# Optimization experiments

Measured on AMD Instinct MI355X. Metric: run time of the kernel, lower is better.

Reference implementation:

```python
import jax, jax.numpy as jnp
import numpy as np

T, H, I, E = 8192, 1024, 2816, 8


def setup_inputs() -> dict:
    key = jax.random.key(0)
    ks = jax.random.split(key, 4)
    x = jax.random.normal(ks[0], (T, H), dtype=jnp.float32)
    router_logits = jax.random.normal(ks[1], (T, E), dtype=jnp.float32)
    # params scaled like trained weights
    w13 = jax.random.normal(ks[2], (E, 2 * I, H), dtype=jnp.float32) * (1.0 / np.sqrt(H))
    w2 = jax.random.normal(ks[3], (E, H, I), dtype=jnp.float32) * (1.0 / np.sqrt(I))
    return {"x": x, "router_logits": router_logits, "w13": w13, "w2": w2, "top_k": 2}


def reference(x, router_logits, w13, w2, top_k):
    """select_experts (softmax scoring, top-k, renormalize) + fused_experts (SiLU-gated MLP per expert, weighted combine)."""
    Ttok, Hd = x.shape
    Ex, twoI, _ = w13.shape
    Id = twoI // 2
    # --- router: softmax -> top_k -> renormalize ---
    probs = jax.nn.softmax(router_logits.astype(jnp.float32), axis=-1)  # [T, E]
    topk_w, topk_ids = jax.lax.top_k(probs, top_k)                      # [T, k]
    topk_w = topk_w / jnp.sum(topk_w, axis=-1, keepdims=True)
    # per-expert combine weight matrix [T, E] (scatter of topk weights)
    comb = jnp.zeros((Ttok, Ex), dtype=x.dtype).at[
        jnp.arange(Ttok)[:, None], topk_ids
    ].add(topk_w.astype(x.dtype))
    # --- expert MLPs: out = sum_e comb[:,e] * (silu(x W1_e^T) * (x W3_e^T)) W2_e^T ---
    out = jnp.zeros_like(x)
    for e in range(Ex):  # small fixed expert count
        gate = x @ w13[e, :Id].T          # [T, I]
        up = x @ w13[e, Id:].T            # [T, I]
        h = jax.nn.silu(gate) * up        # [T, I]
        out = out + comb[:, e:e + 1] * (h @ w2[e].T)  # [T, H]
    return out
```

## Files before the change

### kernel.cpp

```cpp
#include <hip/hip_runtime.h>
#include <hip/hip_bf16.h>

#define T_TOK 8192
#define H_DIM 1024
#define I_DIM 2816
#define E_NUM 8
#define R_TOT (2 * T_TOK)

typedef __hip_bfloat16 bf16;
typedef __attribute__((ext_vector_type(8))) short short8;
typedef __attribute__((ext_vector_type(4))) float floatx4;

__device__ inline unsigned short f2b(float f) {
    bf16 b = __float2bfloat16(f);
    unsigned short u;
    __builtin_memcpy(&u, &b, 2);
    return u;
}

__device__ inline short8 ld_cvt8(const float* p) {
    float4 f0 = *(const float4*)p;
    float4 f1 = *(const float4*)(p + 4);
    short8 r;
    r[0] = (short)f2b(f0.x); r[1] = (short)f2b(f0.y);
    r[2] = (short)f2b(f0.z); r[3] = (short)f2b(f0.w);
    r[4] = (short)f2b(f1.x); r[5] = (short)f2b(f1.y);
    r[6] = (short)f2b(f1.z); r[7] = (short)f2b(f1.w);
    return r;
}

__device__ inline void gl_lds16(const void* g, void* l) {
    __builtin_amdgcn_global_load_lds(
        (const __attribute__((address_space(1))) void*)g,
        (__attribute__((address_space(3))) void*)l, 16, 0, 0);
}


__global__ __launch_bounds__(256) void cvt_bf16_kernel(const float* __restrict__ in,
                                                       bf16* __restrict__ out, int n8) {
    int stride = gridDim.x * blockDim.x;
    for (int i = blockIdx.x * blockDim.x + threadIdx.x; i < n8; i += stride) {
        short8 v = ld_cvt8(in + (size_t)i * 8);
        *(short8*)(out + (size_t)i * 8) = v;
    }
}


__global__ void zero_counts_kernel(int* counts) {
    if (threadIdx.x < E_NUM) counts[threadIdx.x] = 0;
}

__global__ void zero_out_kernel(float* __restrict__ out) {
    size_t i = ((size_t)blockIdx.x * 256 + threadIdx.x) * 4;
    float4 z = {0.0f, 0.0f, 0.0f, 0.0f};
    *(float4*)(out + i) = z;
}

__global__ void router_kernel(const float* __restrict__ logits,
                              int* __restrict__ topk_id,
                              float* __restrict__ topk_w,
                              int* __restrict__ counts) {
    int t = blockIdx.x * blockDim.x + threadIdx.x;
    if (t >= T_TOK) return;
    float l[E_NUM];
#pragma unroll
    for (int e = 0; e < E_NUM; e++) l[e] = logits[t * E_NUM + e];
    int i0 = 0;
#pragma unroll
    for (int e = 1; e < E_NUM; e++)
        if (l[e] > l[i0]) i0 = e;
    int i1 = (i0 == 0) ? 1 : 0;
#pragma unroll
    for (int e = 0; e < E_NUM; e++) {
        if (e == i0 || e == i1) continue;
        if (l[e] > l[i1]) i1 = e;
    }
    float p1 = __expf(l[i1] - l[i0]);
    float w0 = 1.0f / (1.0f + p1);
    float w1 = p1 / (1.0f + p1);
    topk_id[2 * t] = i0;
    topk_id[2 * t + 1] = i1;
    topk_w[2 * t] = w0;
    topk_w[2 * t + 1] = w1;
    atomicAdd(&counts[i0], 1);
    atomicAdd(&counts[i1], 1);
}

__global__ void offsets_kernel(const int* __restrict__ counts,
                               int* __restrict__ offs,
                               int* __restrict__ cursor) {
    if (threadIdx.x == 0 && blockIdx.x == 0) {
        int acc = 0;
        for (int e = 0; e < E_NUM; e++) {
            offs[e] = acc;
            cursor[e] = acc;
            acc += counts[e];
        }
        offs[E_NUM] = acc;
    }
}

__global__ void scatter_kernel(const int* __restrict__ topk_id,
                               const float* __restrict__ topk_w,
                               int* __restrict__ cursor,
                               int* __restrict__ rowtok,
                               float* __restrict__ wrow) {
    int t = blockIdx.x * blockDim.x + threadIdx.x;
    if (t >= T_TOK) return;
#pragma unroll
    for (int j = 0; j < 2; j++) {
        int e = topk_id[2 * t + j];
        int r = atomicAdd(&cursor[e], 1);
        rowtok[r] = t;
        wrow[r] = topk_w[2 * t + j];
    }
}


__global__ __launch_bounds__(256) void gemm1_bf16_kernel(
    const bf16* __restrict__ xb, const bf16* __restrict__ wptr,
    long long wstride, int e_base,
    const int* __restrict__ offs, const int* __restrict__ rowtok,
    bf16* __restrict__ h) {
    const int ei = blockIdx.y >> 6;
    const int e = e_base + ei;
    const int tm = blockIdx.y & 63;
    const int mBeg = offs[e], mEnd = offs[e + 1];
    const int m0 = mBeg + tm * 128;
    if (m0 >= mEnd) return;
    const int n0 = blockIdx.x * 128;

    __shared__ alignas(16) bf16 As[2][128 * 32];
    __shared__ alignas(16) bf16 Bg[2][128 * 32];
    __shared__ alignas(16) bf16 Bu[2][128 * 32];

    const int tid = threadIdx.x;
    const int lane = tid & 63;
    const int wv = tid >> 6;
    const int wr = wv >> 1, wc = wv & 1;

    const int c0 = tid, c1 = tid + 256;
    const int ar0 = c0 >> 2, ks0 = (c0 & 3) * 8;
    const int ar1 = c1 >> 2, ks1 = (c1 & 3) * 8;
    const bf16* aG0 = xb + (size_t)rowtok[min(m0 + ar0, R_TOT - 1)] * H_DIM + ks0;
    const bf16* aG1 = xb + (size_t)rowtok[min(m0 + ar1, R_TOT - 1)] * H_DIM + ks1;
    const bf16* w13e = wptr + (size_t)ei * wstride;
    const bf16* bG0 = w13e + (size_t)(n0 + ar0) * H_DIM + ks0;
    const bf16* bG1 = w13e + (size_t)(n0 + ar1) * H_DIM + ks1;
    const bf16* uG0 = w13e + (size_t)(I_DIM + n0 + ar0) * H_DIM + ks0;
    const bf16* uG1 = w13e + (size_t)(I_DIM + n0 + ar1) * H_DIM + ks1;

    const int wb8 = (wv * 64) * 8;
    const int wb8b = (wv * 64 + 256) * 8;

#define STG1(B, KT)                          \
    gl_lds16(aG0 + (KT), &As[B][wb8]);       \
    gl_lds16(aG1 + (KT), &As[B][wb8b]);      \
    gl_lds16(bG0 + (KT), &Bg[B][wb8]);       \
    gl_lds16(bG1 + (KT), &Bg[B][wb8b]);      \
    gl_lds16(uG0 + (KT), &Bu[B][wb8]);       \
    gl_lds16(uG1 + (KT), &Bu[B][wb8b]);

    floatx4 accG[4][4] = {};
    floatx4 accU[4][4] = {};

    const int lr = lane & 15;
    const int kg = lane >> 4;

    STG1(0, 0);
    __syncthreads();

    int cur = 0;
    for (int kt = 0; kt < H_DIM; kt += 32) {
        if (kt + 32 < H_DIM) { STG1(cur ^ 1, kt + 32); }

        short8 af[4], bgf[4], buf2[4];
#pragma unroll
        for (int i = 0; i < 4; i++)
            af[i] = *(const short8*)(&As[cur][(wr * 64 + i * 16 + lr) * 32 + kg * 8]);
#pragma unroll
        for (int j = 0; j < 4; j++) {
            bgf[j] = *(const short8*)(&Bg[cur][(wc * 64 + j * 16 + lr) * 32 + kg * 8]);
            buf2[j] = *(const short8*)(&Bu[cur][(wc * 64 + j * 16 + lr) * 32 + kg * 8]);
        }
#pragma unroll
        for (int i = 0; i < 4; i++)
#pragma unroll
            for (int j = 0; j < 4; j++) {
                accG[i][j] = __builtin_amdgcn_mfma_f32_16x16x32_bf16(af[i], bgf[j], accG[i][j], 0, 0, 0);
                accU[i][j] = __builtin_amdgcn_mfma_f32_16x16x32_bf16(af[i], buf2[j], accU[i][j], 0, 0, 0);
            }
        __syncthreads();
        cur ^= 1;
    }
#undef STG1

    const int quad = lane >> 4;
#pragma unroll
    for (int i = 0; i < 4; i++) {
        const int grb = m0 + wr * 64 + i * 16 + quad * 4;
#pragma unroll
        for (int j = 0; j < 4; j++) {
            const int gc = n0 + wc * 64 + j * 16 + lr;
#pragma unroll
            for (int v = 0; v < 4; v++) {
                const int gr = grb + v;
                if (gr < mEnd) {
                    float g = accG[i][j][v];
                    float u = accU[i][j][v];
                    float s = g / (1.0f + __expf(-g));
                    h[(size_t)gr * I_DIM + gc] = __float2bfloat16(s * u);
                }
            }
        }
    }
}


__global__ __launch_bounds__(256) void gemm2_bf16_kernel(
    const bf16* __restrict__ hbuf, const bf16* __restrict__ wptr,
    long long wstride, int e_base,
    const int* __restrict__ offs, const int* __restrict__ rowtok,
    const float* __restrict__ wrow, float* __restrict__ out) {
    const int ei = blockIdx.y >> 6;
    const int e = e_base + ei;
    const int tm = blockIdx.y & 63;
    const int mBeg = offs[e], mEnd = offs[e + 1];
    const int m0 = mBeg + tm * 128;
    if (m0 >= mEnd) return;
    const int n0 = blockIdx.x * 128;

    __shared__ alignas(16) bf16 As[2][128 * 32];
    __shared__ alignas(16) bf16 Bs[2][128 * 32];

    const int tid = threadIdx.x;
    const int lane = tid & 63;
    const int wv = tid >> 6;
    const int wr = wv >> 1, wc = wv & 1;

    const int c0 = tid, c1 = tid + 256;
    const int ar0 = c0 >> 2, ks0 = (c0 & 3) * 8;
    const int ar1 = c1 >> 2, ks1 = (c1 & 3) * 8;
    const bf16* aG0 = hbuf + (size_t)min(m0 + ar0, R_TOT - 1) * I_DIM + ks0;
    const bf16* aG1 = hbuf + (size_t)min(m0 + ar1, R_TOT - 1) * I_DIM + ks1;
    const bf16* w2e = wptr + (size_t)ei * wstride;
    const bf16* bG0 = w2e + (size_t)(n0 + ar0) * I_DIM + ks0;
    const bf16* bG1 = w2e + (size_t)(n0 + ar1) * I_DIM + ks1;

    const int wb8 = (wv * 64) * 8;
    const int wb8b = (wv * 64 + 256) * 8;

#define STG2(B, KT)                          \
    gl_lds16(aG0 + (KT), &As[B][wb8]);       \
    gl_lds16(aG1 + (KT), &As[B][wb8b]);      \
    gl_lds16(bG0 + (KT), &Bs[B][wb8]);       \
    gl_lds16(bG1 + (KT), &Bs[B][wb8b]);

    floatx4 acc[4][4] = {};
    const int lr = lane & 15;
    const int kg = lane >> 4;

    STG2(0, 0);
    __syncthreads();

    int cur = 0;
    for (int kt = 0; kt < I_DIM; kt += 32) {
        if (kt + 32 < I_DIM) { STG2(cur ^ 1, kt + 32); }

        short8 af[4], bf_[4];
#pragma unroll
        for (int i = 0; i < 4; i++)
            af[i] = *(const short8*)(&As[cur][(wr * 64 + i * 16 + lr) * 32 + kg * 8]);
#pragma unroll
        for (int j = 0; j < 4; j++)
            bf_[j] = *(const short8*)(&Bs[cur][(wc * 64 + j * 16 + lr) * 32 + kg * 8]);
#pragma unroll
        for (int i = 0; i < 4; i++)
#pragma unroll
            for (int j = 0; j < 4; j++)
                acc[i][j] = __builtin_amdgcn_mfma_f32_16x16x32_bf16(af[i], bf_[j], acc[i][j], 0, 0, 0);
        __syncthreads();
        cur ^= 1;
    }
#undef STG2

    const int quad = lane >> 4;
#pragma unroll
    for (int i = 0; i < 4; i++) {
        const int grb = m0 + wr * 64 + i * 16 + quad * 4;
#pragma unroll
        for (int j = 0; j < 4; j++) {
            const int gc = n0 + wc * 64 + j * 16 + lr;
#pragma unroll
            for (int v = 0; v < 4; v++) {
                const int gr = grb + v;
                if (gr < mEnd) {
                    const int t = rowtok[gr];
                    atomicAdd(&out[(size_t)t * H_DIM + gc], wrow[gr] * acc[i][j][v]);
                }
            }
        }
    }
}


__global__ __launch_bounds__(256) void gemm1_f32_kernel(
    const float* __restrict__ x, const float* __restrict__ w13,
    const int* __restrict__ offs, const int* __restrict__ rowtok,
    bf16* __restrict__ h) {
    const int e = blockIdx.y >> 6;
    const int tm = blockIdx.y & 63;
    const int mBeg = offs[e], mEnd = offs[e + 1];
    const int m0 = mBeg + tm * 128;
    if (m0 >= mEnd) return;
    const int n0 = blockIdx.x * 128;

    __shared__ alignas(16) bf16 As[128 * 32];
    __shared__ alignas(16) bf16 Bg[128 * 32];
    __shared__ alignas(16) bf16 Bu[128 * 32];

    const int tid = threadIdx.x;
    const int lane = tid & 63;
    const int wv = tid >> 6;
    const int wr = wv >> 1, wc = wv & 1;

    const int c0 = tid, c1 = tid + 256;
    const int ar0 = c0 >> 2, ks0 = (c0 & 3) * 8;
    const int ar1 = c1 >> 2, ks1 = (c1 & 3) * 8;
    const int rr0 = min(m0 + ar0, R_TOT - 1);
    const int rr1 = min(m0 + ar1, R_TOT - 1);
    const float* aG0 = x + (size_t)rowtok[rr0] * H_DIM + ks0;
    const float* aG1 = x + (size_t)rowtok[rr1] * H_DIM + ks1;
    const float* w13e = w13 + (size_t)e * (2 * I_DIM) * H_DIM;
    const float* bG0 = w13e + (size_t)(n0 + ar0) * H_DIM + ks0;
    const float* bG1 = w13e + (size_t)(n0 + ar1) * H_DIM + ks1;
    const float* uG0 = w13e + (size_t)(I_DIM + n0 + ar0) * H_DIM + ks0;
    const float* uG1 = w13e + (size_t)(I_DIM + n0 + ar1) * H_DIM + ks1;

    floatx4 accG[4][4] = {};
    floatx4 accU[4][4] = {};

    const int lr = lane & 15;
    const int kg = lane >> 4;

    for (int kt = 0; kt < H_DIM; kt += 32) {
        short8 va0 = ld_cvt8(aG0 + kt);
        short8 va1 = ld_cvt8(aG1 + kt);
        short8 vg0 = ld_cvt8(bG0 + kt);
        short8 vg1 = ld_cvt8(bG1 + kt);
        short8 vu0 = ld_cvt8(uG0 + kt);
        short8 vu1 = ld_cvt8(uG1 + kt);
        __syncthreads();
        *(short8*)(As + c0 * 8) = va0;
        *(short8*)(As + c1 * 8) = va1;
        *(short8*)(Bg + c0 * 8) = vg0;
        *(short8*)(Bg + c1 * 8) = vg1;
        *(short8*)(Bu + c0 * 8) = vu0;
        *(short8*)(Bu + c1 * 8) = vu1;
        __syncthreads();

        short8 af[4], bgf[4], buf2[4];
#pragma unroll
        for (int i = 0; i < 4; i++)
            af[i] = *(const short8*)(As + (wr * 64 + i * 16 + lr) * 32 + kg * 8);
#pragma unroll
        for (int j = 0; j < 4; j++) {
            bgf[j] = *(const short8*)(Bg + (wc * 64 + j * 16 + lr) * 32 + kg * 8);
            buf2[j] = *(const short8*)(Bu + (wc * 64 + j * 16 + lr) * 32 + kg * 8);
        }
#pragma unroll
        for (int i = 0; i < 4; i++)
#pragma unroll
            for (int j = 0; j < 4; j++) {
                accG[i][j] = __builtin_amdgcn_mfma_f32_16x16x32_bf16(af[i], bgf[j], accG[i][j], 0, 0, 0);
                accU[i][j] = __builtin_amdgcn_mfma_f32_16x16x32_bf16(af[i], buf2[j], accU[i][j], 0, 0, 0);
            }
    }

    const int quad = lane >> 4;
#pragma unroll
    for (int i = 0; i < 4; i++) {
        const int grb = m0 + wr * 64 + i * 16 + quad * 4;
#pragma unroll
        for (int j = 0; j < 4; j++) {
            const int gc = n0 + wc * 64 + j * 16 + lr;
#pragma unroll
            for (int v = 0; v < 4; v++) {
                const int gr = grb + v;
                if (gr < mEnd) {
                    float g = accG[i][j][v];
                    float u = accU[i][j][v];
                    float s = g / (1.0f + __expf(-g));
                    h[(size_t)gr * I_DIM + gc] = __float2bfloat16(s * u);
                }
            }
        }
    }
}

__global__ __launch_bounds__(256) void gemm2_f32_kernel(
    const bf16* __restrict__ hbuf, const float* __restrict__ w2,
    const int* __restrict__ offs, const int* __restrict__ rowtok,
    const float* __restrict__ wrow, float* __restrict__ out) {
    const int e = blockIdx.y >> 6;
    const int tm = blockIdx.y & 63;
    const int mBeg = offs[e], mEnd = offs[e + 1];
    const int m0 = mBeg + tm * 128;
    if (m0 >= mEnd) return;
    const int n0 = blockIdx.x * 128;

    __shared__ alignas(16) bf16 As[128 * 32];
    __shared__ alignas(16) bf16 Bs[128 * 32];

    const int tid = threadIdx.x;
    const int lane = tid & 63;
    const int wv = tid >> 6;
    const int wr = wv >> 1, wc = wv & 1;

    const int c0 = tid, c1 = tid + 256;
    const int ar0 = c0 >> 2, ks0 = (c0 & 3) * 8;
    const int ar1 = c1 >> 2, ks1 = (c1 & 3) * 8;
    const bf16* aG0 = hbuf + (size_t)min(m0 + ar0, R_TOT - 1) * I_DIM + ks0;
    const bf16* aG1 = hbuf + (size_t)min(m0 + ar1, R_TOT - 1) * I_DIM + ks1;
    const float* w2e = w2 + (size_t)e * H_DIM * I_DIM;
    const float* bG0 = w2e + (size_t)(n0 + ar0) * I_DIM + ks0;
    const float* bG1 = w2e + (size_t)(n0 + ar1) * I_DIM + ks1;

    floatx4 acc[4][4] = {};
    const int lr = lane & 15;
    const int kg = lane >> 4;

    for (int kt = 0; kt < I_DIM; kt += 32) {
        short8 va0 = *(const short8*)(aG0 + kt);
        short8 va1 = *(const short8*)(aG1 + kt);
        short8 vb0 = ld_cvt8(bG0 + kt);
        short8 vb1 = ld_cvt8(bG1 + kt);
        __syncthreads();
        *(short8*)(As + c0 * 8) = va0;
        *(short8*)(As + c1 * 8) = va1;
        *(short8*)(Bs + c0 * 8) = vb0;
        *(short8*)(Bs + c1 * 8) = vb1;
        __syncthreads();

        short8 af[4], bf_[4];
#pragma unroll
        for (int i = 0; i < 4; i++)
            af[i] = *(const short8*)(As + (wr * 64 + i * 16 + lr) * 32 + kg * 8);
#pragma unroll
        for (int j = 0; j < 4; j++)
            bf_[j] = *(const short8*)(Bs + (wc * 64 + j * 16 + lr) * 32 + kg * 8);
#pragma unroll
        for (int i = 0; i < 4; i++)
#pragma unroll
            for (int j = 0; j < 4; j++)
                acc[i][j] = __builtin_amdgcn_mfma_f32_16x16x32_bf16(af[i], bf_[j], acc[i][j], 0, 0, 0);
    }

    const int quad = lane >> 4;
#pragma unroll
    for (int i = 0; i < 4; i++) {
        const int grb = m0 + wr * 64 + i * 16 + quad * 4;
#pragma unroll
        for (int j = 0; j < 4; j++) {
            const int gc = n0 + wc * 64 + j * 16 + lr;
#pragma unroll
            for (int v = 0; v < 4; v++) {
                const int gr = grb + v;
                if (gr < mEnd) {
                    const int t = rowtok[gr];
                    atomicAdd(&out[(size_t)t * H_DIM + gc], wrow[gr] * acc[i][j][v]);
                }
            }
        }
    }
}


extern "C" void kernel_launch(void* const* d_in, const int* in_sizes, int n_in,
                              void* d_out, int out_size, void* d_ws, size_t ws_size,
                              hipStream_t stream) {
    const float* x = (const float*)d_in[0];
    const float* rl = (const float*)d_in[1];
    const float* w13 = (const float*)d_in[2];
    const float* w2 = (const float*)d_in[3];
    float* out = (float*)d_out;

    char* ws = (char*)d_ws;
    int* counts = (int*)(ws);
    int* offs = (int*)(ws + 256);
    int* cursor = (int*)(ws + 512);
    int* topk_id = (int*)(ws + 1024);
    float* topk_w = (float*)(ws + 1024 + 65536);
    int* rowtok = (int*)(ws + 1024 + 2 * 65536);
    float* wrow = (float*)(ws + 1024 + 3 * 65536);

    const size_t BASE = 1024 + 4 * 65536;
    const size_t H_BYTES = (size_t)R_TOT * I_DIM * 2;
    const size_t XB_BYTES = (size_t)T_TOK * H_DIM * 2;
    const size_t W13_BYTES = (size_t)E_NUM * 2 * I_DIM * H_DIM * 2;
    const size_t W13_SLICE = (size_t)2 * I_DIM * H_DIM * 2;
    const size_t W2_SLICE = (size_t)H_DIM * I_DIM * 2;

    bf16* h = (bf16*)(ws + BASE);
    bf16* xb = (bf16*)(ws + BASE + H_BYTES);
    bf16* wbuf = (bf16*)(ws + BASE + H_BYTES + XB_BYTES);

    const size_t NEED_BULK = BASE + H_BYTES + XB_BYTES + W13_BYTES;
    const size_t NEED_SLICE = BASE + H_BYTES + XB_BYTES + W13_SLICE;

    zero_out_kernel<<<(T_TOK * H_DIM) / (256 * 4), 256, 0, stream>>>(out);
    zero_counts_kernel<<<1, 64, 0, stream>>>(counts);
    router_kernel<<<(T_TOK + 255) / 256, 256, 0, stream>>>(rl, topk_id, topk_w, counts);
    offsets_kernel<<<1, 64, 0, stream>>>(counts, offs, cursor);
    scatter_kernel<<<(T_TOK + 255) / 256, 256, 0, stream>>>(topk_id, topk_w, cursor, rowtok, wrow);

    if (ws_size >= NEED_BULK) {
        cvt_bf16_kernel<<<2048, 256, 0, stream>>>(x, xb, (T_TOK * H_DIM) / 8);
        cvt_bf16_kernel<<<2048, 256, 0, stream>>>(w13, wbuf, (int)(W13_BYTES / 2 / 8));
        gemm1_bf16_kernel<<<dim3(I_DIM / 128, E_NUM * 64), 256, 0, stream>>>(
            xb, wbuf, (long long)2 * I_DIM * H_DIM, 0, offs, rowtok, h);
        cvt_bf16_kernel<<<2048, 256, 0, stream>>>(w2, wbuf, (E_NUM * H_DIM * I_DIM) / 8);
        gemm2_bf16_kernel<<<dim3(H_DIM / 128, E_NUM * 64), 256, 0, stream>>>(
            h, wbuf, (long long)H_DIM * I_DIM, 0, offs, rowtok, wrow, out);
    } else if (ws_size >= NEED_SLICE) {
        cvt_bf16_kernel<<<2048, 256, 0, stream>>>(x, xb, (T_TOK * H_DIM) / 8);
        for (int e = 0; e < E_NUM; e++) {
            cvt_bf16_kernel<<<1024, 256, 0, stream>>>(
                w13 + (size_t)e * 2 * I_DIM * H_DIM, wbuf, (int)(W13_SLICE / 2 / 8));
            gemm1_bf16_kernel<<<dim3(I_DIM / 128, 64), 256, 0, stream>>>(
                xb, wbuf, 0LL, e, offs, rowtok, h);
        }
        for (int e = 0; e < E_NUM; e++) {
            cvt_bf16_kernel<<<1024, 256, 0, stream>>>(
                w2 + (size_t)e * H_DIM * I_DIM, wbuf, (int)(W2_SLICE / 2 / 8));
            gemm2_bf16_kernel<<<dim3(H_DIM / 128, 64), 256, 0, stream>>>(
                h, wbuf, 0LL, e, offs, rowtok, wrow, out);
        }
    } else {
        gemm1_f32_kernel<<<dim3(I_DIM / 128, E_NUM * 64), 256, 0, stream>>>(
            x, w13, offs, rowtok, h);
        gemm2_f32_kernel<<<dim3(H_DIM / 128, E_NUM * 64), 256, 0, stream>>>(
            h, w2, offs, rowtok, wrow, out);
    }
}
```

Baseline: 1.180 ms.

## Enlarge MoE GEMM tiles to 512-thread blocks with swizzled LDS and phased MFMA

Both expert GEMMs now use 512-thread blocks with larger output tiles: 256x128 for the gate/up GEMM and 256x256 for the down GEMM. K steps go from 32 to 64, and shared memory is a 128KB dynamic buffer with an XOR swizzle to reduce bank conflicts. Each K tile is split into four MFMA phases separated by raw barriers, with s_setprio raised around the MFMA bursts. The aim is more operand reuse per global load and better latency hiding. The cost is higher register and LDS pressure, which means one block per CU, and the down GEMM no longer clamps row indices when reading h.

```diff
diff --git a/kernel.cpp b/kernel.cpp
--- a/kernel.cpp
+++ b/kernel.cpp
@@ -35,6 +35,9 @@
         (__attribute__((address_space(3))) void*)l, 16, 0, 0);
 }
 
+#define BARX() do { asm volatile("" ::: "memory"); __builtin_amdgcn_s_barrier(); asm volatile("" ::: "memory"); } while (0)
+#define WAIT_VM0() asm volatile("s_waitcnt vmcnt(0)" ::: "memory")
+
 
 __global__ __launch_bounds__(256) void cvt_bf16_kernel(const float* __restrict__ in,
                                                        bf16* __restrict__ out, int n8) {
@@ -117,85 +120,102 @@
 }
 
 
-__global__ __launch_bounds__(256) void gemm1_bf16_kernel(
+__global__ __launch_bounds__(512) void gemm1_8ph_kernel(
     const bf16* __restrict__ xb, const bf16* __restrict__ wptr,
     long long wstride, int e_base,
     const int* __restrict__ offs, const int* __restrict__ rowtok,
     bf16* __restrict__ h) {
-    const int ei = blockIdx.y >> 6;
+    const int ei = blockIdx.y >> 5;
     const int e = e_base + ei;
-    const int tm = blockIdx.y & 63;
+    const int tm = blockIdx.y & 31;
     const int mBeg = offs[e], mEnd = offs[e + 1];
-    const int m0 = mBeg + tm * 128;
+    const int m0 = mBeg + tm * 256;
     if (m0 >= mEnd) return;
     const int n0 = blockIdx.x * 128;
 
-    __shared__ alignas(16) bf16 As[2][128 * 32];
-    __shared__ alignas(16) bf16 Bg[2][128 * 32];
-    __shared__ alignas(16) bf16 Bu[2][128 * 32];
+    extern __shared__ char smem[];
+    bf16* Alds = (bf16*)smem;
+    bf16* Gl = Alds + 32768;
+    bf16* Ul = Gl + 16384;
 
     const int tid = threadIdx.x;
     const int lane = tid & 63;
     const int wv = tid >> 6;
     const int wr = wv >> 1, wc = wv & 1;
-
-    const int c0 = tid, c1 = tid + 256;
-    const int ar0 = c0 >> 2, ks0 = (c0 & 3) * 8;
-    const int ar1 = c1 >> 2, ks1 = (c1 & 3) * 8;
-    const bf16* aG0 = xb + (size_t)rowtok[min(m0 + ar0, R_TOT - 1)] * H_DIM + ks0;
-    const bf16* aG1 = xb + (size_t)rowtok[min(m0 + ar1, R_TOT - 1)] * H_DIM + ks1;
+    const int lr = lane & 15, kg = lane >> 4;
+    const int swz = lr & 7;
+    const int srow = wv * 8 + (lane >> 3);
+    const int socto = ((lane & 7) ^ (lane >> 3)) * 8;
+    const int dA = wv * 512;
+
     const bf16* w13e = wptr + (size_t)ei * wstride;
-    const bf16* bG0 = w13e + (size_t)(n0 + ar0) * H_DIM + ks0;
-    const bf16* bG1 = w13e + (size_t)(n0 + ar1) * H_DIM + ks1;
-    const bf16* uG0 = w13e + (size_t)(I_DIM + n0 + ar0) * H_DIM + ks0;
-    const bf16* uG1 = w13e + (size_t)(I_DIM + n0 + ar1) * H_DIM + ks1;
-
-    const int wb8 = (wv * 64) * 8;
-    const int wb8b = (wv * 64 + 256) * 8;
-
-#define STG1(B, KT)                          \
-    gl_lds16(aG0 + (KT), &As[B][wb8]);       \
-    gl_lds16(aG1 + (KT), &As[B][wb8b]);      \
-    gl_lds16(bG0 + (KT), &Bg[B][wb8]);       \
-    gl_lds16(bG1 + (KT), &Bg[B][wb8b]);      \
-    gl_lds16(uG0 + (KT), &Bu[B][wb8]);       \
-    gl_lds16(uG1 + (KT), &Bu[B][wb8b]);
+    const bf16* aP[4];
+    const bf16 *gP[2], *uP[2];
+#pragma unroll
+    for (int L = 0; L < 4; L++)
+        aP[L] = xb + (size_t)rowtok[min(m0 + L * 64 + srow, R_TOT - 1)] * H_DIM + socto;
+#pragma unroll
+    for (int L = 0; L < 2; L++) {
+        gP[L] = w13e + (size_t)(n0 + L * 64 + srow) * H_DIM + socto;
+        uP[L] = w13e + (size_t)(I_DIM + n0 + L * 64 + srow) * H_DIM + socto;
+    }
+
+#define STG1(B, KT) do {                                          \
+    gl_lds16(aP[0] + (KT), Alds + (B) * 16384 + 0 * 4096 + dA);   \
+    gl_lds16(aP[1] + (KT), Alds + (B) * 16384 + 1 * 4096 + dA);   \
+    gl_lds16(aP[2] + (KT), Alds + (B) * 16384 + 2 * 4096 + dA);   \
+    gl_lds16(aP[3] + (KT), Alds + (B) * 16384 + 3 * 4096 + dA);   \
+    gl_lds16(gP[0] + (KT), Gl + (B) * 8192 + 0 * 4096 + dA);      \
+    gl_lds16(gP[1] + (KT), Gl + (B) * 8192 + 1 * 4096 + dA);      \
+    gl_lds16(uP[0] + (KT), Ul + (B) * 8192 + 0 * 4096 + dA);      \
+    gl_lds16(uP[1] + (KT), Ul + (B) * 8192 + 1 * 4096 + dA);      \
+} while (0)
 
     floatx4 accG[4][4] = {};
     floatx4 accU[4][4] = {};
-
-    const int lr = lane & 15;
-    const int kg = lane >> 4;
+    const int arl = wr * 64 + lr;
+
+#define PHASE1(ACC, BT, PC) do {                                                          \
+    const bf16* aT = Alds + cur * 16384;                                                  \
+    const bf16* bT = (BT) + cur * 8192;                                                   \
+    short8 af[4][2], bfr[2][2];                                                           \
+    _Pragma("unroll") for (int i = 0; i < 4; i++)                                         \
+    _Pragma("unroll") for (int s = 0; s < 2; s++)                                         \
+        af[i][s] = *(const short8*)(aT + (arl + i * 16) * 64 + (((s * 4 + kg) ^ swz) * 8)); \
+    _Pragma("unroll") for (int j = 0; j < 2; j++)                                         \
+    _Pragma("unroll") for (int s = 0; s < 2; s++)                                         \
+        bfr[j][s] = *(const short8*)(bT + (wc * 64 + (PC) * 32 + j * 16 + lr) * 64 + (((s * 4 + kg) ^ swz) * 8)); \
+    __builtin_amdgcn_s_setprio(1);                                                        \
+    _Pragma("unroll") for (int i = 0; i < 4; i++)                                         \
+    _Pragma("unroll") for (int j = 0; j < 2; j++)                                         \
+    _Pragma("unroll") for (int s = 0; s < 2; s++)                                         \
+        ACC[i][(PC) * 2 + j] = __builtin_amdgcn_mfma_f32_16x16x32_bf16(af[i][s], bfr[j][s], ACC[i][(PC) * 2 + j], 0, 0, 0); \
+    __builtin_amdgcn_s_setprio(0);                                                        \
+} while (0)
 
     STG1(0, 0);
-    __syncthreads();
+    WAIT_VM0();
+    BARX();
 
     int cur = 0;
-    for (int kt = 0; kt < H_DIM; kt += 32) {
-        if (kt + 32 < H_DIM) { STG1(cur ^ 1, kt + 32); }
-
-        short8 af[4], bgf[4], buf2[4];
-#pragma unroll
-        for (int i = 0; i < 4; i++)
-            af[i] = *(const short8*)(&As[cur][(wr * 64 + i * 16 + lr) * 32 + kg * 8]);
-#pragma unroll
-        for (int j = 0; j < 4; j++) {
-            bgf[j] = *(const short8*)(&Bg[cur][(wc * 64 + j * 16 + lr) * 32 + kg * 8]);
-            buf2[j] = *(const short8*)(&Bu[cur][(wc * 64 + j * 16 + lr) * 32 + kg * 8]);
-        }
-#pragma unroll
-        for (int i = 0; i < 4; i++)
-#pragma unroll
-            for (int j = 0; j < 4; j++) {
-                accG[i][j] = __builtin_amdgcn_mfma_f32_16x16x32_bf16(af[i], bgf[j], accG[i][j], 0, 0, 0);
-                accU[i][j] = __builtin_amdgcn_mfma_f32_16x16x32_bf16(af[i], buf2[j], accU[i][j], 0, 0, 0);
-            }
-        __syncthreads();
+    const int NT = H_DIM / 64;
+    for (int t = 0; t < NT; ++t) {
+        if (t + 1 < NT) STG1(cur ^ 1, (t + 1) * 64);
+        PHASE1(accG, Gl, 0);
+        BARX();
+        PHASE1(accG, Gl, 1);
+        BARX();
+        PHASE1(accU, Ul, 0);
+        BARX();
+        PHASE1(accU, Ul, 1);
+        WAIT_VM0();
+        BARX();
         cur ^= 1;
     }
 #undef STG1
-
-    const int quad = lane >> 4;
+#undef PHASE1
+
+    const int quad = kg;
 #pragma unroll
     for (int i = 0; i < 4; i++) {
         const int grb = m0 + wr * 64 + i * 16 + quad * 4;
@@ -217,77 +237,99 @@
 }
 
 
-__global__ __launch_bounds__(256) void gemm2_bf16_kernel(
+__global__ __launch_bounds__(512) void gemm2_8ph_kernel(
     const bf16* __restrict__ hbuf, const bf16* __restrict__ wptr,
     long long wstride, int e_base,
     const int* __restrict__ offs, const int* __restrict__ rowtok,
     const float* __restrict__ wrow, float* __restrict__ out) {
-    const int ei = blockIdx.y >> 6;
+    const int ei = blockIdx.y >> 5;
     const int e = e_base + ei;
-    const int tm = blockIdx.y & 63;
+    const int tm = blockIdx.y & 31;
     const int mBeg = offs[e], mEnd = offs[e + 1];
-    const int m0 = mBeg + tm * 128;
+    const int m0 = mBeg + tm * 256;
     if (m0 >= mEnd) return;
-    const int n0 = blockIdx.x * 128;
-
-    __shared__ alignas(16) bf16 As[2][128 * 32];
-    __shared__ alignas(16) bf16 Bs[2][128 * 32];
+    const int n0 = blockIdx.x * 256;
+
+    extern __shared__ char smem[];
+    bf16* Alds = (bf16*)smem;
+    bf16* Blds = Alds + 32768;
 
     const int tid = threadIdx.x;
     const int lane = tid & 63;
     const int wv = tid >> 6;
-    const int wr = wv >> 1, wc = wv & 1;
-
-    const int c0 = tid, c1 = tid + 256;
-    const int ar0 = c0 >> 2, ks0 = (c0 & 3) * 8;
-    const int ar1 = c1 >> 2, ks1 = (c1 & 3) * 8;
-    const bf16* aG0 = hbuf + (size_t)min(m0 + ar0, R_TOT - 1) * I_DIM + ks0;
-    const bf16* aG1 = hbuf + (size_t)min(m0 + ar1, R_TOT - 1) * I_DIM + ks1;
+    const int wr = wv >> 2, wc = wv & 3;
+    const int lr = lane & 15, kg = lane >> 4;
+    const int swz = lr & 7;
+    const int srow = wv * 8 + (lane >> 3);
+    const int socto = ((lane & 7) ^ (lane >> 3)) * 8;
+    const int dA = wv * 512;
+
     const bf16* w2e = wptr + (size_t)ei * wstride;
-    const bf16* bG0 = w2e + (size_t)(n0 + ar0) * I_DIM + ks0;
-    const bf16* bG1 = w2e + (size_t)(n0 + ar1) * I_DIM + ks1;
-
-    const int wb8 = (wv * 64) * 8;
-    const int wb8b = (wv * 64 + 256) * 8;
-
-#define STG2(B, KT)                          \
-    gl_lds16(aG0 + (KT), &As[B][wb8]);       \
-    gl_lds16(aG1 + (KT), &As[B][wb8b]);      \
-    gl_lds16(bG0 + (KT), &Bs[B][wb8]);       \
-    gl_lds16(bG1 + (KT), &Bs[B][wb8b]);
-
-    floatx4 acc[4][4] = {};
-    const int lr = lane & 15;
-    const int kg = lane >> 4;
+    const bf16* aP[4];
+    const bf16* bP[4];
+#pragma unroll
+    for (int L = 0; L < 4; L++) {
+        aP[L] = hbuf + (size_t)(m0 + L * 64 + srow) * I_DIM + socto;
+        bP[L] = w2e + (size_t)(n0 + L * 64 + srow) * I_DIM + socto;
+    }
+
+#define STG2(B, KT) do {                                          \
+    gl_lds16(aP[0] + (KT), Alds + (B) * 16384 + 0 * 4096 + dA);   \
+    gl_lds16(aP[1] + (KT), Alds + (B) * 16384 + 1 * 4096 + dA);   \
+    gl_lds16(aP[2] + (KT), Alds + (B) * 16384 + 2 * 4096 + dA);   \
+    gl_lds16(aP[3] + (KT), Alds + (B) * 16384 + 3 * 4096 + dA);   \
+    gl_lds16(bP[0] + (KT), Blds + (B) * 16384 + 0 * 4096 + dA);   \
+    gl_lds16(bP[1] + (KT), Blds + (B) * 16384 + 1 * 4096 + dA);   \
+    gl_lds16(bP[2] + (KT), Blds + (B) * 16384 + 2 * 4096 + dA);   \
+    gl_lds16(bP[3] + (KT), Blds + (B) * 16384 + 3 * 4096 + dA);   \
+} while (0)
+
+    floatx4 acc[8][4] = {};
+
+#define PHASE2(PR, PC) do {                                                               \
+    const bf16* aT = Alds + cur * 16384;                                                  \
+    const bf16* bT = Blds + cur * 16384;                                                  \
+    short8 af[4][2], bfr[2][2];                                                           \
+    _Pragma("unroll") for (int i2 = 0; i2 < 4; i2++)                                      \
+    _Pragma("unroll") for (int s = 0; s < 2; s++)                                         \
+        af[i2][s] = *(const short8*)(aT + (wr * 128 + (PR) * 64 + i2 * 16 + lr) * 64 + (((s * 4 + kg) ^ swz) * 8)); \
+    _Pragma("unroll") for (int j = 0; j < 2; j++)                                         \
+    _Pragma("unroll") for (int s = 0; s < 2; s++)                                         \
+        bfr[j][s] = *(const short8*)(bT + (wc * 64 + (PC) * 32 + j * 16 + lr) * 64 + (((s * 4 + kg) ^ swz) * 8)); \
+    __builtin_amdgcn_s_setprio(1);                                                        \
+    _Pragma("unroll") for (int i2 = 0; i2 < 4; i2++)                                      \
+    _Pragma("unroll") for (int j = 0; j < 2; j++)                                         \
+    _Pragma("unroll") for (int s = 0; s < 2; s++)                                         \
+        acc[(PR) * 4 + i2][(PC) * 2 + j] = __builtin_amdgcn_mfma_f32_16x16x32_bf16(af[i2][s], bfr[j][s], acc[(PR) * 4 + i2][(PC) * 2 + j], 0, 0, 0); \
+    __builtin_amdgcn_s_setprio(0);                                                        \
+} while (0)
 
     STG2(0, 0);
-    __syncthreads();
+    WAIT_VM0();
+    BARX();
 
     int cur = 0;
-    for (int kt = 0; kt < I_DIM; kt += 32) {
-        if (kt + 32 < I_DIM) { STG2(cur ^ 1, kt + 32); }
-
-        short8 af[4], bf_[4];
-#pragma unroll
-        for (int i = 0; i < 4; i++)
-            af[i] = *(const short8*)(&As[cur][(wr * 64 + i * 16 + lr) * 32 + kg * 8]);
-#pragma unroll
-        for (int j = 0; j < 4; j++)
-            bf_[j] = *(const short8*)(&Bs[cur][(wc * 64 + j * 16 + lr) * 32 + kg * 8]);
-#pragma unroll
-        for (int i = 0; i < 4; i++)
-#pragma unroll
-            for (int j = 0; j < 4; j++)
-                acc[i][j] = __builtin_amdgcn_mfma_f32_16x16x32_bf16(af[i], bf_[j], acc[i][j], 0, 0, 0);
-        __syncthreads();
+    const int NT = I_DIM / 64;
+    for (int t = 0; t < NT; ++t) {
+        if (t + 1 < NT) STG2(cur ^ 1, (t + 1) * 64);
+        PHASE2(0, 0);
+        BARX();
+        PHASE2(0, 1);
+        BARX();
+        PHASE2(1, 0);
+        BARX();
+        PHASE2(1, 1);
+        WAIT_VM0();
+        BARX();
         cur ^= 1;
     }
 #undef STG2
-
-    const int quad = lane >> 4;
-#pragma unroll
-    for (int i = 0; i < 4; i++) {
-        const int grb = m0 + wr * 64 + i * 16 + quad * 4;
+#undef PHASE2
+
+    const int quad = kg;
+#pragma unroll
+    for (int i = 0; i < 8; i++) {
+        const int grb = m0 + wr * 128 + i * 16 + quad * 4;
 #pragma unroll
         for (int j = 0; j < 4; j++) {
             const int gc = n0 + wc * 64 + j * 16 + lr;
@@ -508,6 +550,11 @@
     const size_t NEED_BULK = BASE + H_BYTES + XB_BYTES + W13_BYTES;
     const size_t NEED_SLICE = BASE + H_BYTES + XB_BYTES + W13_SLICE;
 
+    hipFuncSetAttribute(reinterpret_cast<const void*>(gemm1_8ph_kernel),
+                        hipFuncAttributeMaxDynamicSharedMemorySize, 131072);
+    hipFuncSetAttribute(reinterpret_cast<const void*>(gemm2_8ph_kernel),
+                        hipFuncAttributeMaxDynamicSharedMemorySize, 131072);
+
     zero_out_kernel<<<(T_TOK * H_DIM) / (256 * 4), 256, 0, stream>>>(out);
     zero_counts_kernel<<<1, 64, 0, stream>>>(counts);
     router_kernel<<<(T_TOK + 255) / 256, 256, 0, stream>>>(rl, topk_id, topk_w, counts);
@@ -517,23 +564,23 @@
     if (ws_size >= NEED_BULK) {
         cvt_bf16_kernel<<<2048, 256, 0, stream>>>(x, xb, (T_TOK * H_DIM) / 8);
         cvt_bf16_kernel<<<2048, 256, 0, stream>>>(w13, wbuf, (int)(W13_BYTES / 2 / 8));
-        gemm1_bf16_kernel<<<dim3(I_DIM / 128, E_NUM * 64), 256, 0, stream>>>(
+        gemm1_8ph_kernel<<<dim3(I_DIM / 128, E_NUM * 32), 512, 131072, stream>>>(
             xb, wbuf, (long long)2 * I_DIM * H_DIM, 0, offs, rowtok, h);
         cvt_bf16_kernel<<<2048, 256, 0, stream>>>(w2, wbuf, (E_NUM * H_DIM * I_DIM) / 8);
-        gemm2_bf16_kernel<<<dim3(H_DIM / 128, E_NUM * 64), 256, 0, stream>>>(
+        gemm2_8ph_kernel<<<dim3(H_DIM / 256, E_NUM * 32), 512, 131072, stream>>>(
             h, wbuf, (long long)H_DIM * I_DIM, 0, offs, rowtok, wrow, out);
     } else if (ws_size >= NEED_SLICE) {
         cvt_bf16_kernel<<<2048, 256, 0, stream>>>(x, xb, (T_TOK * H_DIM) / 8);
         for (int e = 0; e < E_NUM; e++) {
             cvt_bf16_kernel<<<1024, 256, 0, stream>>>(
                 w13 + (size_t)e * 2 * I_DIM * H_DIM, wbuf, (int)(W13_SLICE / 2 / 8));
-            gemm1_bf16_kernel<<<dim3(I_DIM / 128, 64), 256, 0, stream>>>(
+            gemm1_8ph_kernel<<<dim3(I_DIM / 128, 32), 512, 131072, stream>>>(
                 xb, wbuf, 0LL, e, offs, rowtok, h);
         }
         for (int e = 0; e < E_NUM; e++) {
             cvt_bf16_kernel<<<1024, 256, 0, stream>>>(
                 w2 + (size_t)e * H_DIM * I_DIM, wbuf, (int)(W2_SLICE / 2 / 8));
-            gemm2_bf16_kernel<<<dim3(H_DIM / 128, 64), 256, 0, stream>>>(
+            gemm2_8ph_kernel<<<dim3(H_DIM / 256, 32), 512, 131072, stream>>>(
                 h, wbuf, 0LL, e, offs, rowtok, wrow, out);
         }
     } else {
```

After: 1.062 ms. 10.0% less time.
